# Performance work log

Hardware: AMD Instinct MI355X
Metric: run time of the kernel (lower is better)

## Reference

```python
import jax, jax.numpy as jnp
import numpy as np

L = 10           # outer iterations (module arg L -> sinkhorn n_iter)
N_INNER = 1      # n_inner_iter=1 in SinkhornLoss.forward
EPS = 1.0        # entropic regularization epsilon


def setup_inputs() -> dict:
    key = jax.random.key(0)
    kx, ky = jax.random.split(key)
    x = jax.random.normal(kx, (8192, 32), dtype=jnp.float32)
    y = jax.random.normal(ky, (8192, 32), dtype=jnp.float32)
    return {"x": x, "y": y}


def _sinkhorn_loss(x, y):
    n, m = x.shape[0], y.shape[0]
    # sqeuclidean cdist: [n, m]
    C = (x * x).sum(1)[:, None] + (y * y).sum(1)[None, :] - 2.0 * (x @ y.T)
    # uniform marginals mu = 1/n, nu = 1/m (mu=None, nu=None in source)
    logmu = -jnp.log(jnp.asarray(n, C.dtype))
    lognu = -jnp.log(jnp.asarray(m, C.dtype))
    f0 = jnp.zeros((n,), C.dtype)
    g0 = jnp.zeros((m,), C.dtype)

    def body(carry, _):
        f, g = carry
        # log-domain Sinkhorn updates (stable logsumexp form)
        f = EPS * (logmu - jax.nn.logsumexp((g[None, :] - C) / EPS, axis=1))
        g = EPS * (lognu - jax.nn.logsumexp((f[:, None] - C) / EPS, axis=0))
        return (f, g), None

    (f, g), _ = jax.lax.scan(body, (f0, g0), None, length=L * N_INNER)
    gamma = jnp.exp((f[:, None] + g[None, :] - C) / EPS)  # transport plan [n, m]
    return jnp.sum(C * gamma)  # min_cost = <C, gamma>


def reference(x, y):
    return _sinkhorn_loss(x, y)
```

## Files before the change

kernel.cpp:

```cpp
#include <hip/hip_runtime.h>
#include <math.h>


#define KDIM 32
#define NPS 32
#define NSL_LOSS 16
#define LOG2E 1.44269504088896340736f
#define LN2 0.69314718055994530942f

typedef short short8 __attribute__((ext_vector_type(8)));
typedef float f32x4 __attribute__((ext_vector_type(4)));

__device__ __forceinline__ unsigned short f2bf(float f) {
    unsigned int u = __float_as_uint(f);
    u += 0x7FFF + ((u >> 16) & 1);
    return (unsigned short)(u >> 16);
}
__device__ __forceinline__ float bf2f(unsigned short b) {
    return __uint_as_float(((unsigned int)b) << 16);
}

__global__ void prep_split(const float* __restrict__ x, const float* __restrict__ y,
                           int nelem,
                           unsigned short* __restrict__ xh, unsigned short* __restrict__ xl,
                           unsigned short* __restrict__ yh, unsigned short* __restrict__ yl) {
    int i4 = (blockIdx.x * 256 + threadIdx.x) * 4;
    if (i4 >= 2 * nelem) return;
    const float* src; unsigned short* dh; unsigned short* dl; int off; float sc;
    if (i4 < nelem) { src = x; dh = xh; dl = xl; off = i4; sc = 2.0f * LOG2E; }
    else            { src = y; dh = yh; dl = yl; off = i4 - nelem; sc = 1.0f; }
    float4 v = *(const float4*)(src + off);
    v.x *= sc; v.y *= sc; v.z *= sc; v.w *= sc;
    ushort4 h, l;
    h.x = f2bf(v.x); l.x = f2bf(v.x - bf2f(h.x));
    h.y = f2bf(v.y); l.y = f2bf(v.y - bf2f(h.y));
    h.z = f2bf(v.z); l.z = f2bf(v.z - bf2f(h.z));
    h.w = f2bf(v.w); l.w = f2bf(v.w - bf2f(h.w));
    *(ushort4*)(dh + off) = h;
    *(ushort4*)(dl + off) = l;
}

__global__ void prep_sq(const float* __restrict__ x, const float* __restrict__ y,
                        int n, float* __restrict__ xsq, float* __restrict__ ysq,
                        float* __restrict__ pb0) {
    int i = blockIdx.x * blockDim.x + threadIdx.x;
    if (i >= 2 * n) return;
    const float* src = (i < n) ? x : y;
    int r = (i < n) ? i : i - n;
    const float4* p = (const float4*)(src + (size_t)r * KDIM);
    float s = 0.f;
#pragma unroll
    for (int q = 0; q < 8; ++q) {
        float4 v = p[q];
        s += v.x * v.x + v.y * v.y + v.z * v.z + v.w * v.w;
    }
    if (i < n) xsq[r] = s;
    else { ysq[r] = s; pb0[r] = __builtin_amdgcn_exp2f(-LOG2E * s); }
}

__global__ __launch_bounds__(256, 4) void sink_pass(
    const unsigned short* __restrict__ Ah, const unsigned short* __restrict__ Alo,
    const unsigned short* __restrict__ Bh, const unsigned short* __restrict__ Blo,
    const float* __restrict__ pb_direct,
    const float* __restrict__ psum_in,
    float* __restrict__ psum_out, int n, float inv_n) {
    __shared__ float pbl[256];
    __shared__ float red[4][64][17];

    const int tid = threadIdx.x;
    const int w = tid >> 6, lane = tid & 63;
    const int mrow = lane & 15, quad = lane >> 4, koff = quad * 8;
    const int i0 = (blockIdx.x * 4 + w) * 64;
    const int jbeg = blockIdx.y * (n / NPS);

    {
        int c = jbeg + tid;
        float b;
        if (pb_direct) {
            b = pb_direct[c];
        } else {
            float s = 0.f;
#pragma unroll
            for (int k = 0; k < NPS; ++k) s += psum_in[(size_t)k * n + c];
            b = inv_n / s;
        }
        pbl[tid] = b;
    }

    short8 aH[4], aL[4];
#pragma unroll
    for (int t = 0; t < 4; ++t) {
        size_t rb = (size_t)(i0 + t * 16 + mrow) * KDIM + koff;
        aH[t] = *(const short8*)(Ah + rb);
        aL[t] = *(const short8*)(Alo + rb);
    }
    __syncthreads();

    float rs[16];
#pragma unroll
    for (int q = 0; q < 16; ++q) rs[q] = 0.f;

    auto ldB = [&](int jt, short8* bh, short8* bl, float* pb) {
        const int j0 = jbeg + jt * 32;
#pragma unroll
        for (int u = 0; u < 2; ++u) {
            size_t rb = (size_t)(j0 + u * 16 + mrow) * KDIM + koff;
            bh[u] = *(const short8*)(Bh + rb);
            bl[u] = *(const short8*)(Blo + rb);
            pb[u] = pbl[jt * 32 + u * 16 + mrow];
        }
    };
    auto compute = [&](short8* bh, short8* bl, float* pb) {
#pragma unroll
        for (int t = 0; t < 4; ++t)
#pragma unroll
            for (int u = 0; u < 2; ++u) {
                f32x4 z = {0.f, 0.f, 0.f, 0.f};
                z = __builtin_amdgcn_mfma_f32_16x16x32_bf16(aH[t], bh[u], z, 0, 0, 0);
                z = __builtin_amdgcn_mfma_f32_16x16x32_bf16(aH[t], bl[u], z, 0, 0, 0);
                z = __builtin_amdgcn_mfma_f32_16x16x32_bf16(aL[t], bh[u], z, 0, 0, 0);
#pragma unroll
                for (int r = 0; r < 4; ++r)
                    rs[t * 4 + r] = fmaf(__builtin_amdgcn_exp2f(z[r]), pb[u], rs[t * 4 + r]);
            }
    };

    const int JT = (n / NPS) / 32;
    short8 bh0[2], bl0[2], bh1[2], bl1[2];
    float pb0v[2], pb1v[2];
    ldB(0, bh0, bl0, pb0v);
    for (int jt = 0; jt < JT; jt += 2) {
        ldB(jt + 1, bh1, bl1, pb1v);
        compute(bh0, bl0, pb0v);
        if (jt + 2 < JT) ldB(jt + 2, bh0, bl0, pb0v);
        compute(bh1, bl1, pb1v);
    }

#pragma unroll
    for (int t = 0; t < 4; ++t)
#pragma unroll
        for (int r = 0; r < 4; ++r)
            red[w][t * 16 + quad * 4 + r][mrow] = rs[t * 4 + r];
    __syncthreads();
    {
        int w2 = tid >> 6, row = tid & 63;
        float s = 0.f;
#pragma unroll
        for (int c = 0; c < 16; ++c) s += red[w2][row][c];
        psum_out[(size_t)blockIdx.y * n + (blockIdx.x * 4 + w2) * 64 + row] = s;
    }
}

__global__ __launch_bounds__(256, 4) void sink_loss(
    const unsigned short* __restrict__ Xh, const unsigned short* __restrict__ Xl,
    const unsigned short* __restrict__ Yh, const unsigned short* __restrict__ Yl,
    const float* __restrict__ apsum, const float* __restrict__ bpsum,
    const float* __restrict__ xsq, const float* __restrict__ ysq,
    float* __restrict__ partials, int n, float inv_n) {
    __shared__ float pbL[512];
    __shared__ float ysl[512];
    __shared__ float pal[128];
    __shared__ float xsl[128];
    __shared__ float red[256];

    const int tid = threadIdx.x;
    const int w = tid >> 6, lane = tid & 63;
    const int mrow = lane & 15, quad = lane >> 4, koff = quad * 8;
    const int i0 = (blockIdx.x * 4 + w) * 32;
    const int jbeg = blockIdx.y * (n / NSL_LOSS);

#pragma unroll
    for (int h = 0; h < 2; ++h) {
        int c = tid + h * 256;
        int j = jbeg + c;
        float s = 0.f;
#pragma unroll
        for (int k = 0; k < NPS; ++k) s += bpsum[(size_t)k * n + j];
        pbL[c] = inv_n / s;
        ysl[c] = ysq[j];
    }
    if (tid < 128) {
        int i = blockIdx.x * 128 + tid;
        float s = 0.f;
#pragma unroll
        for (int k = 0; k < NPS; ++k) s += apsum[(size_t)k * n + i];
        pal[tid] = inv_n / s;
        xsl[tid] = xsq[i];
    }

    short8 aH[2], aL[2];
#pragma unroll
    for (int t = 0; t < 2; ++t) {
        size_t rb = (size_t)(i0 + t * 16 + mrow) * KDIM + koff;
        aH[t] = *(const short8*)(Xh + rb);
        aL[t] = *(const short8*)(Xl + rb);
    }
    __syncthreads();

    float pa[8], xs[8];
#pragma unroll
    for (int t = 0; t < 2; ++t)
#pragma unroll
        for (int r = 0; r < 4; ++r) {
            int rl = w * 32 + t * 16 + quad * 4 + r;
            pa[t * 4 + r] = pal[rl];
            xs[t * 4 + r] = xsl[rl];
        }

    float acc = 0.f;

    auto ldB = [&](int jt, short8* bh, short8* bl, float* pb, float* ysv) {
#pragma unroll
        for (int u = 0; u < 2; ++u) {
            int cl = jt * 32 + u * 16 + mrow;
            size_t rb = (size_t)(jbeg + cl) * KDIM + koff;
            bh[u] = *(const short8*)(Yh + rb);
            bl[u] = *(const short8*)(Yl + rb);
            pb[u] = pbL[cl];
            ysv[u] = ysl[cl];
        }
    };
    auto compute = [&](short8* bh, short8* bl, float* pb, float* ysv) {
#pragma unroll
        for (int t = 0; t < 2; ++t)
#pragma unroll
            for (int u = 0; u < 2; ++u) {
                f32x4 z = {0.f, 0.f, 0.f, 0.f};
                z = __builtin_amdgcn_mfma_f32_16x16x32_bf16(aH[t], bh[u], z, 0, 0, 0);
                z = __builtin_amdgcn_mfma_f32_16x16x32_bf16(aH[t], bl[u], z, 0, 0, 0);
                z = __builtin_amdgcn_mfma_f32_16x16x32_bf16(aL[t], bh[u], z, 0, 0, 0);
#pragma unroll
                for (int r = 0; r < 4; ++r) {
                    float dd = z[r];
                    float e = __builtin_amdgcn_exp2f(dd) * (pa[t * 4 + r] * pb[u]);
                    float cst = fmaf(dd, -LN2, xs[t * 4 + r] + ysv[u]);
                    acc = fmaf(cst, e, acc);
                }
            }
    };

    const int JT = (n / NSL_LOSS) / 32;
    short8 bh0[2], bl0[2], bh1[2], bl1[2];
    float pb0v[2], pb1v[2], ys0v[2], ys1v[2];
    ldB(0, bh0, bl0, pb0v, ys0v);
    for (int jt = 0; jt < JT; jt += 2) {
        ldB(jt + 1, bh1, bl1, pb1v, ys1v);
        compute(bh0, bl0, pb0v, ys0v);
        if (jt + 2 < JT) ldB(jt + 2, bh0, bl0, pb0v, ys0v);
        compute(bh1, bl1, pb1v, ys1v);
    }

    red[tid] = acc;
    __syncthreads();
#pragma unroll
    for (int s = 128; s > 0; s >>= 1) {
        if (tid < s) red[tid] += red[tid + s];
        __syncthreads();
    }
    if (tid == 0) partials[blockIdx.y * gridDim.x + blockIdx.x] = red[0];
}

__global__ void sink_reduce(const float* __restrict__ p, int nb,
                            float* __restrict__ out) {
    __shared__ float red[256];
    int tid = threadIdx.x;
    float v = 0.f;
    for (int i = tid; i < nb; i += 256) v += p[i];
    red[tid] = v;
    __syncthreads();
#pragma unroll
    for (int s = 128; s > 0; s >>= 1) {
        if (tid < s) red[tid] += red[tid + s];
        __syncthreads();
    }
    if (tid == 0) out[0] = red[0];
}

extern "C" void kernel_launch(void* const* d_in, const int* in_sizes, int n_in,
                              void* d_out, int out_size, void* d_ws, size_t ws_size,
                              hipStream_t stream) {
    const float* x = (const float*)d_in[0];
    const float* y = (const float*)d_in[1];
    const int n = in_sizes[0] / KDIM;
    const int nelem = n * KDIM;
    const float inv_n = 1.0f / (float)n;

    float* ws = (float*)d_ws;
    float* xsq   = ws;
    float* ysq   = ws + n;
    float* pb0   = ws + 2 * n;
    float* apsum = ws + 3 * n;
    float* bpsum = ws + (3 + NPS) * n;
    float* part  = ws + (3 + 2 * NPS) * n;
    unsigned short* us = (unsigned short*)(ws + (4 + 2 * NPS) * n);
    unsigned short* xh = us;
    unsigned short* xl = us + nelem;
    unsigned short* yh = us + 2 * nelem;
    unsigned short* yl = us + 3 * nelem;

    dim3 pgrid(n / 256, NPS);
    dim3 lgrid(n / 128, NSL_LOSS);

    prep_split<<<(2 * nelem / 4 + 255) / 256, 256, 0, stream>>>(x, y, nelem, xh, xl, yh, yl);
    prep_sq<<<(2 * n + 255) / 256, 256, 0, stream>>>(x, y, n, xsq, ysq, pb0);

    sink_pass<<<pgrid, 256, 0, stream>>>(xh, xl, yh, yl, pb0, nullptr, apsum, n, inv_n);
    sink_pass<<<pgrid, 256, 0, stream>>>(yh, yl, xh, xl, nullptr, apsum, bpsum, n, inv_n);
    for (int t = 1; t < 10; ++t) {
        sink_pass<<<pgrid, 256, 0, stream>>>(xh, xl, yh, yl, nullptr, bpsum, apsum, n, inv_n);
        sink_pass<<<pgrid, 256, 0, stream>>>(yh, yl, xh, xl, nullptr, apsum, bpsum, n, inv_n);
    }
    sink_loss<<<lgrid, 256, 0, stream>>>(xh, xl, yh, yl, apsum, bpsum, xsq, ysq, part, n, inv_n);
    sink_reduce<<<1, 256, 0, stream>>>(part, (n / 128) * NSL_LOSS, (float*)d_out);
}
```

Before: 406.0 us.

## Transpose partial-sum layout and halve row tile per wave for more occupancy

Stores the per-slice partial row sums transposed ([row][slice]), so each consumer reads 32 contiguous floats with float4 loads instead of 32 strided loads. Each wave now covers 32 rows instead of 64, the grid doubles to n/128 blocks, and launch bounds ask for 8 blocks per CU to raise occupancy. The loss kernel uses the same 32-slice split. The trade is half the A-fragment reuse per B load, so more B traffic and more partial sums per row, and the transposed writes are strided.

```diff
diff --git a/kernel.cpp b/kernel.cpp
--- a/kernel.cpp
+++ b/kernel.cpp
@@ -4,7 +4,6 @@
 
 #define KDIM 32
 #define NPS 32
-#define NSL_LOSS 16
 #define LOG2E 1.44269504088896340736f
 #define LN2 0.69314718055994530942f
 
@@ -58,47 +57,51 @@
     else { ysq[r] = s; pb0[r] = __builtin_amdgcn_exp2f(-LOG2E * s); }
 }
 
-__global__ __launch_bounds__(256, 4) void sink_pass(
+__global__ __launch_bounds__(256, 8) void sink_pass(
     const unsigned short* __restrict__ Ah, const unsigned short* __restrict__ Alo,
     const unsigned short* __restrict__ Bh, const unsigned short* __restrict__ Blo,
     const float* __restrict__ pb_direct,
-    const float* __restrict__ psum_in,
-    float* __restrict__ psum_out, int n, float inv_n) {
+    const float* __restrict__ psumT_in,
+    float* __restrict__ psumT_out, int n, float inv_n) {
     __shared__ float pbl[256];
-    __shared__ float red[4][64][17];
+    __shared__ float red[4][32][17];
 
     const int tid = threadIdx.x;
     const int w = tid >> 6, lane = tid & 63;
     const int mrow = lane & 15, quad = lane >> 4, koff = quad * 8;
-    const int i0 = (blockIdx.x * 4 + w) * 64;
+    const int i0 = (blockIdx.x * 4 + w) * 32;
     const int jbeg = blockIdx.y * (n / NPS);
 
     {
-        int c = jbeg + tid;
+        int j = jbeg + tid;
         float b;
         if (pb_direct) {
-            b = pb_direct[c];
+            b = pb_direct[j];
         } else {
+            const float4* p = (const float4*)(psumT_in + (size_t)j * NPS);
             float s = 0.f;
 #pragma unroll
-            for (int k = 0; k < NPS; ++k) s += psum_in[(size_t)k * n + c];
+            for (int q = 0; q < NPS / 4; ++q) {
+                float4 v = p[q];
+                s += v.x + v.y + v.z + v.w;
+            }
             b = inv_n / s;
         }
         pbl[tid] = b;
     }
 
-    short8 aH[4], aL[4];
-#pragma unroll
-    for (int t = 0; t < 4; ++t) {
+    short8 aH[2], aL[2];
+#pragma unroll
+    for (int t = 0; t < 2; ++t) {
         size_t rb = (size_t)(i0 + t * 16 + mrow) * KDIM + koff;
         aH[t] = *(const short8*)(Ah + rb);
         aL[t] = *(const short8*)(Alo + rb);
     }
     __syncthreads();
 
-    float rs[16];
-#pragma unroll
-    for (int q = 0; q < 16; ++q) rs[q] = 0.f;
+    float rs[8];
+#pragma unroll
+    for (int q = 0; q < 8; ++q) rs[q] = 0.f;
 
     auto ldB = [&](int jt, short8* bh, short8* bl, float* pb) {
         const int j0 = jbeg + jt * 32;
@@ -112,7 +115,7 @@
     };
     auto compute = [&](short8* bh, short8* bl, float* pb) {
 #pragma unroll
-        for (int t = 0; t < 4; ++t)
+        for (int t = 0; t < 2; ++t)
 #pragma unroll
             for (int u = 0; u < 2; ++u) {
                 f32x4 z = {0.f, 0.f, 0.f, 0.f};
@@ -137,28 +140,29 @@
     }
 
 #pragma unroll
-    for (int t = 0; t < 4; ++t)
+    for (int t = 0; t < 2; ++t)
 #pragma unroll
         for (int r = 0; r < 4; ++r)
             red[w][t * 16 + quad * 4 + r][mrow] = rs[t * 4 + r];
     __syncthreads();
-    {
-        int w2 = tid >> 6, row = tid & 63;
+    if (tid < 128) {
+        int w2 = tid >> 5, row = tid & 31;
         float s = 0.f;
 #pragma unroll
         for (int c = 0; c < 16; ++c) s += red[w2][row][c];
-        psum_out[(size_t)blockIdx.y * n + (blockIdx.x * 4 + w2) * 64 + row] = s;
-    }
-}
-
-__global__ __launch_bounds__(256, 4) void sink_loss(
+        int R = blockIdx.x * 128 + w2 * 32 + row;
+        psumT_out[(size_t)R * NPS + blockIdx.y] = s;
+    }
+}
+
+__global__ __launch_bounds__(256, 8) void sink_loss(
     const unsigned short* __restrict__ Xh, const unsigned short* __restrict__ Xl,
     const unsigned short* __restrict__ Yh, const unsigned short* __restrict__ Yl,
-    const float* __restrict__ apsum, const float* __restrict__ bpsum,
+    const float* __restrict__ apsumT, const float* __restrict__ bpsumT,
     const float* __restrict__ xsq, const float* __restrict__ ysq,
     float* __restrict__ partials, int n, float inv_n) {
-    __shared__ float pbL[512];
-    __shared__ float ysl[512];
+    __shared__ float pbL[256];
+    __shared__ float ysl[256];
     __shared__ float pal[128];
     __shared__ float xsl[128];
     __shared__ float red[256];
@@ -167,23 +171,29 @@
     const int w = tid >> 6, lane = tid & 63;
     const int mrow = lane & 15, quad = lane >> 4, koff = quad * 8;
     const int i0 = (blockIdx.x * 4 + w) * 32;
-    const int jbeg = blockIdx.y * (n / NSL_LOSS);
-
-#pragma unroll
-    for (int h = 0; h < 2; ++h) {
-        int c = tid + h * 256;
-        int j = jbeg + c;
+    const int jbeg = blockIdx.y * (n / NPS);
+
+    {
+        int j = jbeg + tid;
+        const float4* p = (const float4*)(bpsumT + (size_t)j * NPS);
         float s = 0.f;
 #pragma unroll
-        for (int k = 0; k < NPS; ++k) s += bpsum[(size_t)k * n + j];
-        pbL[c] = inv_n / s;
-        ysl[c] = ysq[j];
+        for (int q = 0; q < NPS / 4; ++q) {
+            float4 v = p[q];
+            s += v.x + v.y + v.z + v.w;
+        }
+        pbL[tid] = inv_n / s;
+        ysl[tid] = ysq[j];
     }
     if (tid < 128) {
         int i = blockIdx.x * 128 + tid;
+        const float4* p = (const float4*)(apsumT + (size_t)i * NPS);
         float s = 0.f;
 #pragma unroll
-        for (int k = 0; k < NPS; ++k) s += apsum[(size_t)k * n + i];
+        for (int q = 0; q < NPS / 4; ++q) {
+            float4 v = p[q];
+            s += v.x + v.y + v.z + v.w;
+        }
         pal[tid] = inv_n / s;
         xsl[tid] = xsq[i];
     }
@@ -239,7 +249,7 @@
             }
     };
 
-    const int JT = (n / NSL_LOSS) / 32;
+    const int JT = (n / NPS) / 32;
     short8 bh0[2], bl0[2], bh1[2], bl1[2];
     float pb0v[2], pb1v[2], ys0v[2], ys1v[2];
     ldB(0, bh0, bl0, pb0v, ys0v);
@@ -286,30 +296,29 @@
     const float inv_n = 1.0f / (float)n;
 
     float* ws = (float*)d_ws;
-    float* xsq   = ws;
-    float* ysq   = ws + n;
-    float* pb0   = ws + 2 * n;
-    float* apsum = ws + 3 * n;
-    float* bpsum = ws + (3 + NPS) * n;
-    float* part  = ws + (3 + 2 * NPS) * n;
+    float* xsq    = ws;
+    float* ysq    = ws + n;
+    float* pb0    = ws + 2 * n;
+    float* apsumT = ws + 3 * n;
+    float* bpsumT = ws + (3 + NPS) * n;
+    float* part   = ws + (3 + 2 * NPS) * n;
     unsigned short* us = (unsigned short*)(ws + (4 + 2 * NPS) * n);
     unsigned short* xh = us;
     unsigned short* xl = us + nelem;
     unsigned short* yh = us + 2 * nelem;
     unsigned short* yl = us + 3 * nelem;
 
-    dim3 pgrid(n / 256, NPS);
-    dim3 lgrid(n / 128, NSL_LOSS);
+    dim3 grid(n / 128, NPS);
 
     prep_split<<<(2 * nelem / 4 + 255) / 256, 256, 0, stream>>>(x, y, nelem, xh, xl, yh, yl);
     prep_sq<<<(2 * n + 255) / 256, 256, 0, stream>>>(x, y, n, xsq, ysq, pb0);
 
-    sink_pass<<<pgrid, 256, 0, stream>>>(xh, xl, yh, yl, pb0, nullptr, apsum, n, inv_n);
-    sink_pass<<<pgrid, 256, 0, stream>>>(yh, yl, xh, xl, nullptr, apsum, bpsum, n, inv_n);
+    sink_pass<<<grid, 256, 0, stream>>>(xh, xl, yh, yl, pb0, nullptr, apsumT, n, inv_n);
+    sink_pass<<<grid, 256, 0, stream>>>(yh, yl, xh, xl, nullptr, apsumT, bpsumT, n, inv_n);
     for (int t = 1; t < 10; ++t) {
-        sink_pass<<<pgrid, 256, 0, stream>>>(xh, xl, yh, yl, nullptr, bpsum, apsum, n, inv_n);
-        sink_pass<<<pgrid, 256, 0, stream>>>(yh, yl, xh, xl, nullptr, apsum, bpsum, n, inv_n);
-    }
-    sink_loss<<<lgrid, 256, 0, stream>>>(xh, xl, yh, yl, apsum, bpsum, xsq, ysq, part, n, inv_n);
-    sink_reduce<<<1, 256, 0, stream>>>(part, (n / 128) * NSL_LOSS, (float*)d_out);
-}
+        sink_pass<<<grid, 256, 0, stream>>>(xh, xl, yh, yl, nullptr, bpsumT, apsumT, n, inv_n);
+        sink_pass<<<grid, 256, 0, stream>>>(yh, yl, xh, xl, nullptr, apsumT, bpsumT, n, inv_n);
+    }
+    sink_loss<<<grid, 256, 0, stream>>>(xh, xl, yh, yl, apsumT, bpsumT, xsq, ysq, part, n, inv_n);
+    sink_reduce<<<1, 256, 0, stream>>>(part, (n / 128) * NPS, (float*)d_out);
+}
```

Measured after the change: 1.395 ms. 3.44x slower.
